# Performance work log

Measured on AMD Instinct MI355X. Metric: run time of the kernel, lower is better.

The kernel has to match this reference:

```python
import jax, jax.numpy as jnp
import numpy as np

B, N, D = 4, 2048, 128
H = 4
HD = D // H          # 32
RL = 4               # rl_dim
BETA = 1.0
TEMPER = 1.0
LN_EPS = 1e-5


def _leaky(x, slope=0.01):
    return jnp.where(x > 0, x, slope * x)


def setup_inputs() -> dict:
    key = jax.random.key(0)
    ks = jax.random.split(key, 12)
    s = 0.05
    return {
        "h":    jax.random.normal(ks[0], (B, N, D), jnp.float32),
        "rh":   jax.random.normal(ks[1], (B, N, RL), jnp.float32),
        "Wl":   jax.random.normal(ks[2], (D, D), jnp.float32) * s,   # linear_l weight [out,in]
        "Wr":   jax.random.normal(ks[3], (D, D), jnp.float32) * s,   # linear_r weight
        "al":   jax.random.normal(ks[4], (HD,), jnp.float32) * s,    # att_l weight (Linear(HD,1))
        "ar":   jax.random.normal(ks[5], (HD,), jnp.float32) * s,    # att_r weight
        "Wrs":  jax.random.normal(ks[6], (RL * H, RL), jnp.float32) * s,  # r_source weight
        "Wrt":  jax.random.normal(ks[7], (RL * H, RL), jnp.float32) * s,  # r_target weight
        "Wf":   jax.random.normal(ks[8], (D, D), jnp.float32) * s,   # linear_final weight
        "ln_g": jnp.ones((D,), jnp.float32),
        "ln_b": jnp.zeros((D,), jnp.float32),
    }


def reference(h, rh, Wl, Wr, al, ar, Wrs, Wrt, Wf, ln_g, ln_b):
    b, n, d = h.shape
    # projections -> [B, H, N, HD]
    fl = (h @ Wl.T).reshape(b, n, H, HD).transpose(0, 2, 1, 3)
    fr = (h @ Wr.T).reshape(b, n, H, HD).transpose(0, 2, 1, 3)
    # rank-1 additive attention scores
    sl = _leaky(fl) @ al                      # [B, H, N]
    sr = _leaky(fr) @ ar                      # [B, H, N]
    score = sl[..., :, None] + sr[..., None, :]  # [B, H, N, N]
    # relational bias: r_k @ r_q
    r_k = (rh @ Wrs.T).reshape(b, n, H, RL).transpose(0, 2, 1, 3)  # [B,H,N,RL]
    r_q = (rh @ Wrt.T).reshape(b, n, H, RL).transpose(0, 2, 3, 1)  # [B,H,RL,N]
    score = score + BETA * jnp.einsum('bhnr,bhrm->bhnm', r_k, r_q)
    attn = jax.nn.softmax(score / TEMPER, axis=-1)
    # context
    ctx = jnp.einsum('bhnm,bhmd->bhnd', attn, fr)  # [B,H,N,HD]
    h_sa = ctx.transpose(0, 2, 1, 3).reshape(b, n, d)
    fh = h_sa @ Wf.T
    # residual + LayerNorm
    x = h + fh
    mu = jnp.mean(x, axis=-1, keepdims=True)
    var = jnp.mean(jnp.square(x - mu), axis=-1, keepdims=True)
    return (x - mu) * jax.lax.rsqrt(var + LN_EPS) * ln_g + ln_b
```

## Files before the change

### kernel.cpp

```cpp
#include <hip/hip_runtime.h>

#define NN 2048
#define DD 128
#define HH 4

typedef __attribute__((ext_vector_type(8))) short short8;
typedef __attribute__((ext_vector_type(16))) float f32x16;
typedef __attribute__((ext_vector_type(4))) unsigned uint4v;

static __device__ __forceinline__ unsigned cvtpk(float lo, float hi) {
  unsigned r;
  asm("v_cvt_pk_bf16_f32 %0, %1, %2" : "=v"(r) : "v"(lo), "v"(hi));
  return r;
}
static __device__ __forceinline__ void plswap(unsigned& a, unsigned& b) {
  asm("v_permlane32_swap_b32 %0, %1" : "+v"(a), "+v"(b));
}
static __device__ __forceinline__ float dot4(float4 a, float4 b) {
  return a.x * b.x + a.y * b.y + a.z * b.z + a.w * b.w;
}

__global__ __launch_bounds__(256) void k1_proj(
    const float* __restrict__ h, const float* __restrict__ Wr,
    const float* __restrict__ ar, short* __restrict__ Vt,
    float* __restrict__ sr) {
  __shared__ short wr_s[DD * DD];
  __shared__ short h_s[32 * DD];
  const int t = threadIdx.x;
  const int lane = t & 63, wv = t >> 6;
  const int b = blockIdx.x >> 6;
  const int j0 = (blockIdx.x & 63) * 32;
  {
    const int d = t >> 1, c0 = (t & 1) * 8;
    const float* src = Wr + d * DD + c0 * 8;
#pragma unroll
    for (int c = 0; c < 8; ++c) {
      const float4 x = *(const float4*)(src + c * 8);
      const float4 y = *(const float4*)(src + c * 8 + 4);
      uint4v v = {cvtpk(x.x, x.y), cvtpk(x.z, x.w), cvtpk(y.x, y.y), cvtpk(y.z, y.w)};
      *(uint4v*)(wr_s + d * DD + (((c0 + c) ^ (d & 7)) << 3)) = v;
    }
  }
  {
    const int j = t >> 3, c0 = (t & 7) * 2;
    const float* src = h + (size_t)(b * NN + j0 + j) * DD + c0 * 8;
#pragma unroll
    for (int c = 0; c < 2; ++c) {
      const float4 x = *(const float4*)(src + c * 8);
      const float4 y = *(const float4*)(src + c * 8 + 4);
      uint4v v = {cvtpk(x.x, x.y), cvtpk(x.z, x.w), cvtpk(y.x, y.y), cvtpk(y.z, y.w)};
      *(uint4v*)(h_s + j * DD + (((c0 + c) ^ (j & 7)) << 3)) = v;
    }
  }
  __syncthreads();
  const int l31 = lane & 31, kg = lane >> 5;
  const int rowA = wv * 32 + l31;
  f32x16 acc = {0, 0, 0, 0, 0, 0, 0, 0, 0, 0, 0, 0, 0, 0, 0, 0};
#pragma unroll
  for (int ks = 0; ks < 8; ++ks) {
    const int ch = ks * 2 + kg;
    const short8 a = *(const short8*)(wr_s + rowA * DD + ((ch ^ (rowA & 7)) << 3));
    const short8 bb = *(const short8*)(h_s + l31 * DD + ((ch ^ (l31 & 7)) << 3));
    acc = __builtin_amdgcn_mfma_f32_32x32x16_bf16(a, bb, acc, 0, 0, 0);
  }
  const int hi4 = kg * 4;
  float4 arv[4];
#pragma unroll
  for (int q = 0; q < 4; ++q) arv[q] = *(const float4*)(ar + q * 8 + hi4);
  float srp = 0.f;
  short* vrow = Vt + (size_t)(b * DD + wv * 32) * NN + j0 + l31;
#pragma unroll
  for (int r = 0; r < 16; ++r) {
    const int dloc = (r & 3) + 8 * (r >> 2) + hi4;
    const float v = acc[r];
    const float lv = v > 0.f ? v : 0.01f * v;
    const float arc =
        (r & 3) == 0 ? arv[r >> 2].x : (r & 3) == 1 ? arv[r >> 2].y : (r & 3) == 2 ? arv[r >> 2].z : arv[r >> 2].w;
    srp += lv * arc;
    vrow[(size_t)dloc * NN] = (short)cvtpk(v, v);
  }
  srp += __shfl_xor(srp, 32);
  if (lane < 32) sr[(b * HH + wv) * NN + j0 + lane] = srp;
}

__global__ __launch_bounds__(256) void k2_attn(
    const float* __restrict__ rh, const float* __restrict__ Wrs,
    const float* __restrict__ Wrt, const float* __restrict__ sr,
    const short* __restrict__ Vt, float* __restrict__ h_sa) {
  __shared__ short rqsr_s[NN * 8];
  __shared__ float4 redA[2][4][64];
  __shared__ float redL[2][64];
  __shared__ float tbuf[2][32 * 36];
  const int t = threadIdx.x;
  const int lane = t & 63, wv = t >> 6;
  const int strip = wv >> 1, jh = wv & 1;
  const int bh = blockIdx.y, b = bh >> 2, head = bh & 3;
  const int i0 = blockIdx.x * 64 + strip * 32;
  const int l31 = lane & 31, kg = lane >> 5;

  const float4 wt0 = *(const float4*)(Wrt + (head * 4 + 0) * 4);
  const float4 wt1 = *(const float4*)(Wrt + (head * 4 + 1) * 4);
  const float4 wt2 = *(const float4*)(Wrt + (head * 4 + 2) * 4);
  const float4 wt3 = *(const float4*)(Wrt + (head * 4 + 3) * 4);
#pragma unroll
  for (int q = 0; q < 8; ++q) {
    const int j = q * 256 + t;
    const float4 r4 = *(const float4*)(rh + (size_t)(b * NN + j) * 4);
    const float srj = sr[bh * NN + j];
    uint4v v = {cvtpk(dot4(r4, wt0), dot4(r4, wt1)), cvtpk(dot4(r4, wt2), dot4(r4, wt3)),
                cvtpk(srj, 0.f), 0u};
    *(uint4v*)(rqsr_s + j * 8) = v;
  }
  uint4v bk = {0u, 0u, 0u, 0u};
  if (lane < 32) {
    const float4 r4 = *(const float4*)(rh + (size_t)(b * NN + i0 + l31) * 4);
    const float4 ws0 = *(const float4*)(Wrs + (head * 4 + 0) * 4);
    const float4 ws1 = *(const float4*)(Wrs + (head * 4 + 1) * 4);
    const float4 ws2 = *(const float4*)(Wrs + (head * 4 + 2) * 4);
    const float4 ws3 = *(const float4*)(Wrs + (head * 4 + 3) * 4);
    bk[0] = cvtpk(dot4(r4, ws0), dot4(r4, ws1));
    bk[1] = cvtpk(dot4(r4, ws2), dot4(r4, ws3));
    bk[2] = cvtpk(1.f, 0.f);
  }
  const short8 bkf = __builtin_bit_cast(short8, bk);
  __syncthreads();

  const short* vtb = Vt + (size_t)bh * 32 * NN + (size_t)l31 * NN;
  const f32x16 zero = {0, 0, 0, 0, 0, 0, 0, 0, 0, 0, 0, 0, 0, 0, 0, 0};
  f32x16 acc = zero;
  float lsum = 0.f;
  const int jbase = jh * 1024;
#pragma unroll 2
  for (int jj = 0; jj < 1024; jj += 32) {
    const int j0w = jbase + jj;
    uint4v aqu = *(const uint4v*)(rqsr_s + (j0w + l31) * 8);
    if (lane >= 32) { aqu[0] = 0u; aqu[1] = 0u; aqu[2] = 0u; aqu[3] = 0u; }
    const short8 aq = __builtin_bit_cast(short8, aqu);
    const f32x16 sc = __builtin_amdgcn_mfma_f32_32x32x16_bf16(aq, bkf, zero, 0, 0, 0);
    float e[16];
#pragma unroll
    for (int r = 0; r < 16; ++r) {
      e[r] = __expf(sc[r]);
      lsum += e[r];
    }
    unsigned d0 = cvtpk(e[0], e[1]), d1 = cvtpk(e[2], e[3]);
    unsigned d2 = cvtpk(e[4], e[5]), d3 = cvtpk(e[6], e[7]);
    unsigned d4 = cvtpk(e[8], e[9]), d5 = cvtpk(e[10], e[11]);
    unsigned d6 = cvtpk(e[12], e[13]), d7 = cvtpk(e[14], e[15]);
    plswap(d0, d2);
    plswap(d1, d3);
    plswap(d4, d6);
    plswap(d5, d7);
    uint4v b0u = {d0, d1, d2, d3};
    uint4v b1u = {d4, d5, d6, d7};
    const short8 p0 = __builtin_bit_cast(short8, b0u);
    const short8 p1 = __builtin_bit_cast(short8, b1u);
    const short8 va0 = *(const short8*)(vtb + j0w + kg * 8);
    const short8 va1 = *(const short8*)(vtb + j0w + 16 + kg * 8);
    acc = __builtin_amdgcn_mfma_f32_32x32x16_bf16(va0, p0, acc, 0, 0, 0);
    acc = __builtin_amdgcn_mfma_f32_32x32x16_bf16(va1, p1, acc, 0, 0, 0);
  }
  lsum += __shfl_xor(lsum, 32);
  if (jh == 1) {
#pragma unroll
    for (int rg = 0; rg < 4; ++rg)
      redA[strip][rg][lane] = make_float4(acc[rg * 4], acc[rg * 4 + 1], acc[rg * 4 + 2], acc[rg * 4 + 3]);
    redL[strip][lane] = lsum;
  }
  __syncthreads();
  if (jh == 0) {
#pragma unroll
    for (int rg = 0; rg < 4; ++rg) {
      const float4 o = redA[strip][rg][lane];
      acc[rg * 4] += o.x;
      acc[rg * 4 + 1] += o.y;
      acc[rg * 4 + 2] += o.z;
      acc[rg * 4 + 3] += o.w;
    }
    lsum += redL[strip][lane];
    const float linv = 1.f / lsum;
    const int hi4 = kg * 4;
#pragma unroll
    for (int r = 0; r < 16; ++r) {
      const int dloc = (r & 3) + 8 * (r >> 2) + hi4;
      tbuf[strip][l31 * 36 + dloc] = acc[r] * linv;
    }
  }
  __syncthreads();
  if (jh == 0) {
    const int il = lane >> 1, hf = lane & 1;
    const float* tp = &tbuf[strip][il * 36 + hf * 16];
    float* op = h_sa + (size_t)(b * NN + i0 + il) * DD + head * 32 + hf * 16;
#pragma unroll
    for (int qq = 0; qq < 4; ++qq) *(float4*)(op + qq * 4) = *(const float4*)(tp + qq * 4);
  }
}

__global__ __launch_bounds__(256) void k3_final(
    const float* __restrict__ h_sa, const float* __restrict__ h,
    const float* __restrict__ Wf, const float* __restrict__ ln_g,
    const float* __restrict__ ln_b, float* __restrict__ out) {
  __shared__ float2 redln[4][32];
  __shared__ float2 fin[32];
  const int t = threadIdx.x, lane = t & 63, wv = t >> 6;
  const int l31 = lane & 31, kg = lane >> 5;
  const int rbase = blockIdx.x * 32, c0 = wv * 32;
  f32x16 acc = {0, 0, 0, 0, 0, 0, 0, 0, 0, 0, 0, 0, 0, 0, 0, 0};
  const float* ap0 = h_sa + (size_t)(rbase + l31) * DD;
  const float* bp0 = Wf + (size_t)(c0 + l31) * DD;
#pragma unroll
  for (int ks = 0; ks < 8; ++ks) {
    const int ko = ks * 16 + kg * 8;
    const float4 a0 = *(const float4*)(ap0 + ko);
    const float4 a1 = *(const float4*)(ap0 + ko + 4);
    const float4 b0 = *(const float4*)(bp0 + ko);
    const float4 b1 = *(const float4*)(bp0 + ko + 4);
    uint4v au = {cvtpk(a0.x, a0.y), cvtpk(a0.z, a0.w), cvtpk(a1.x, a1.y), cvtpk(a1.z, a1.w)};
    uint4v bu = {cvtpk(b0.x, b0.y), cvtpk(b0.z, b0.w), cvtpk(b1.x, b1.y), cvtpk(b1.z, b1.w)};
    acc = __builtin_amdgcn_mfma_f32_32x32x16_bf16(__builtin_bit_cast(short8, au),
                                                  __builtin_bit_cast(short8, bu), acc, 0, 0, 0);
  }
  const int hi4 = kg * 4;
  float x[16];
#pragma unroll
  for (int r = 0; r < 16; ++r) {
    const int row = (r & 3) + 8 * (r >> 2) + hi4;
    x[r] = acc[r] + h[(size_t)(rbase + row) * DD + c0 + l31];
    float a = x[r], bsq = x[r] * x[r];
#pragma unroll
    for (int o = 1; o < 32; o <<= 1) {
      a += __shfl_xor(a, o);
      bsq += __shfl_xor(bsq, o);
    }
    if (l31 == 0) redln[wv][row] = make_float2(a, bsq);
  }
  __syncthreads();
  if (wv == 0 && lane < 32) {
    float ss = 0.f, qq = 0.f;
#pragma unroll
    for (int w = 0; w < 4; ++w) {
      const float2 p = redln[w][lane];
      ss += p.x;
      qq += p.y;
    }
    const float mu = ss * (1.f / 128.f);
    const float var = qq * (1.f / 128.f) - mu * mu;
    fin[lane] = make_float2(mu, rsqrtf(var + 1e-5f));
  }
  __syncthreads();
  const float g = ln_g[c0 + l31], bb = ln_b[c0 + l31];
#pragma unroll
  for (int r = 0; r < 16; ++r) {
    const int row = (r & 3) + 8 * (r >> 2) + hi4;
    const float2 f = fin[row];
    out[(size_t)(rbase + row) * DD + c0 + l31] = (x[r] - f.x) * f.y * g + bb;
  }
}

extern "C" void kernel_launch(void* const* d_in, const int* in_sizes, int n_in,
                              void* d_out, int out_size, void* d_ws, size_t ws_size,
                              hipStream_t stream) {
  (void)in_sizes; (void)n_in; (void)out_size; (void)ws_size;
  const float* h = (const float*)d_in[0];
  const float* rh = (const float*)d_in[1];
  const float* Wr = (const float*)d_in[3];
  const float* ar = (const float*)d_in[5];
  const float* Wrs = (const float*)d_in[6];
  const float* Wrt = (const float*)d_in[7];
  const float* Wf = (const float*)d_in[8];
  const float* ln_g = (const float*)d_in[9];
  const float* ln_b = (const float*)d_in[10];
  float* out = (float*)d_out;

  char* ws = (char*)d_ws;
  short* Vt = (short*)ws;
  float* sr = (float*)(ws + (2u << 20));
  float* h_sa = (float*)(ws + (2u << 20) + (256u << 10));

  hipLaunchKernelGGL(k1_proj, dim3(256), dim3(256), 0, stream, h, Wr, ar, Vt, sr);
  hipLaunchKernelGGL(k2_attn, dim3(32, 16), dim3(256), 0, stream, rh, Wrs, Wrt, sr, Vt, h_sa);
  hipLaunchKernelGGL(k3_final, dim3(256), dim3(256), 0, stream, h_sa, h, Wf, ln_g, ln_b, out);
}
```

Measured before the change: 110.4 us.

## Precompute packed rq/sr in projection kernel and split attention keys across four waves

```diff
diff --git a/kernel.cpp b/kernel.cpp
--- a/kernel.cpp
+++ b/kernel.cpp
@@ -3,6 +3,7 @@
 #define NN 2048
 #define DD 128
 #define HH 4
+#define L2E 1.44269504088896f
 
 typedef __attribute__((ext_vector_type(8))) short short8;
 typedef __attribute__((ext_vector_type(16))) float f32x16;
@@ -22,8 +23,9 @@
 
 __global__ __launch_bounds__(256) void k1_proj(
     const float* __restrict__ h, const float* __restrict__ Wr,
-    const float* __restrict__ ar, short* __restrict__ Vt,
-    float* __restrict__ sr) {
+    const float* __restrict__ ar, const float* __restrict__ rh,
+    const float* __restrict__ Wrt, short* __restrict__ Vt,
+    short* __restrict__ rqsr) {
   __shared__ short wr_s[DD * DD];
   __shared__ short h_s[32 * DD];
   const int t = threadIdx.x;
@@ -80,37 +82,33 @@
     vrow[(size_t)dloc * NN] = (short)cvtpk(v, v);
   }
   srp += __shfl_xor(srp, 32);
-  if (lane < 32) sr[(b * HH + wv) * NN + j0 + lane] = srp;
-}
-
-__global__ __launch_bounds__(256) void k2_attn(
+  if (lane < 32) {
+    const int j = j0 + lane;
+    const float4 r4 = *(const float4*)(rh + (size_t)(b * NN + j) * 4);
+    const float4 wt0 = *(const float4*)(Wrt + (wv * 4 + 0) * 4);
+    const float4 wt1 = *(const float4*)(Wrt + (wv * 4 + 1) * 4);
+    const float4 wt2 = *(const float4*)(Wrt + (wv * 4 + 2) * 4);
+    const float4 wt3 = *(const float4*)(Wrt + (wv * 4 + 3) * 4);
+    uint4v v = {cvtpk(L2E * dot4(r4, wt0), L2E * dot4(r4, wt1)),
+                cvtpk(L2E * dot4(r4, wt2), L2E * dot4(r4, wt3)),
+                cvtpk(L2E * srp, 0.f), 0u};
+    *(uint4v*)(rqsr + ((size_t)(b * HH + wv) * NN + j) * 8) = v;
+  }
+}
+
+__global__ __launch_bounds__(512) void k2_attn(
     const float* __restrict__ rh, const float* __restrict__ Wrs,
-    const float* __restrict__ Wrt, const float* __restrict__ sr,
-    const short* __restrict__ Vt, float* __restrict__ h_sa) {
-  __shared__ short rqsr_s[NN * 8];
-  __shared__ float4 redA[2][4][64];
-  __shared__ float redL[2][64];
+    const short* __restrict__ rqsr, const short* __restrict__ Vt,
+    float* __restrict__ h_sa) {
+  __shared__ float red[2][3][64 * 17];
   __shared__ float tbuf[2][32 * 36];
   const int t = threadIdx.x;
   const int lane = t & 63, wv = t >> 6;
-  const int strip = wv >> 1, jh = wv & 1;
+  const int strip = wv >> 2, jh = wv & 3;
   const int bh = blockIdx.y, b = bh >> 2, head = bh & 3;
   const int i0 = blockIdx.x * 64 + strip * 32;
   const int l31 = lane & 31, kg = lane >> 5;
 
-  const float4 wt0 = *(const float4*)(Wrt + (head * 4 + 0) * 4);
-  const float4 wt1 = *(const float4*)(Wrt + (head * 4 + 1) * 4);
-  const float4 wt2 = *(const float4*)(Wrt + (head * 4 + 2) * 4);
-  const float4 wt3 = *(const float4*)(Wrt + (head * 4 + 3) * 4);
-#pragma unroll
-  for (int q = 0; q < 8; ++q) {
-    const int j = q * 256 + t;
-    const float4 r4 = *(const float4*)(rh + (size_t)(b * NN + j) * 4);
-    const float srj = sr[bh * NN + j];
-    uint4v v = {cvtpk(dot4(r4, wt0), dot4(r4, wt1)), cvtpk(dot4(r4, wt2), dot4(r4, wt3)),
-                cvtpk(srj, 0.f), 0u};
-    *(uint4v*)(rqsr_s + j * 8) = v;
-  }
   uint4v bk = {0u, 0u, 0u, 0u};
   if (lane < 32) {
     const float4 r4 = *(const float4*)(rh + (size_t)(b * NN + i0 + l31) * 4);
@@ -123,26 +121,25 @@
     bk[2] = cvtpk(1.f, 0.f);
   }
   const short8 bkf = __builtin_bit_cast(short8, bk);
-  __syncthreads();
-
-  const short* vtb = Vt + (size_t)bh * 32 * NN + (size_t)l31 * NN;
+
+  const short* vtb = Vt + (size_t)bh * 32 * NN + (size_t)l31 * NN + jh * 512;
+  const short* aqp = rqsr + ((size_t)bh * NN + jh * 512 + l31) * 8;
   const f32x16 zero = {0, 0, 0, 0, 0, 0, 0, 0, 0, 0, 0, 0, 0, 0, 0, 0};
   f32x16 acc = zero;
   float lsum = 0.f;
-  const int jbase = jh * 1024;
-#pragma unroll 2
-  for (int jj = 0; jj < 1024; jj += 32) {
-    const int j0w = jbase + jj;
-    uint4v aqu = *(const uint4v*)(rqsr_s + (j0w + l31) * 8);
-    if (lane >= 32) { aqu[0] = 0u; aqu[1] = 0u; aqu[2] = 0u; aqu[3] = 0u; }
+#pragma unroll 4
+  for (int jj = 0; jj < 512; jj += 32) {
+    const uint4v aqu = *(const uint4v*)(aqp + (size_t)jj * 8);
     const short8 aq = __builtin_bit_cast(short8, aqu);
     const f32x16 sc = __builtin_amdgcn_mfma_f32_32x32x16_bf16(aq, bkf, zero, 0, 0, 0);
     float e[16];
 #pragma unroll
-    for (int r = 0; r < 16; ++r) {
-      e[r] = __expf(sc[r]);
-      lsum += e[r];
-    }
+    for (int r = 0; r < 16; ++r) e[r] = exp2f(sc[r]);
+    const float s0 = (e[0] + e[1]) + (e[2] + e[3]);
+    const float s1 = (e[4] + e[5]) + (e[6] + e[7]);
+    const float s2 = (e[8] + e[9]) + (e[10] + e[11]);
+    const float s3 = (e[12] + e[13]) + (e[14] + e[15]);
+    lsum += (s0 + s1) + (s2 + s3);
     unsigned d0 = cvtpk(e[0], e[1]), d1 = cvtpk(e[2], e[3]);
     unsigned d2 = cvtpk(e[4], e[5]), d3 = cvtpk(e[6], e[7]);
     unsigned d4 = cvtpk(e[8], e[9]), d5 = cvtpk(e[10], e[11]);
@@ -155,29 +152,27 @@
     uint4v b1u = {d4, d5, d6, d7};
     const short8 p0 = __builtin_bit_cast(short8, b0u);
     const short8 p1 = __builtin_bit_cast(short8, b1u);
-    const short8 va0 = *(const short8*)(vtb + j0w + kg * 8);
-    const short8 va1 = *(const short8*)(vtb + j0w + 16 + kg * 8);
+    const short8 va0 = *(const short8*)(vtb + jj + kg * 8);
+    const short8 va1 = *(const short8*)(vtb + jj + 16 + kg * 8);
     acc = __builtin_amdgcn_mfma_f32_32x32x16_bf16(va0, p0, acc, 0, 0, 0);
     acc = __builtin_amdgcn_mfma_f32_32x32x16_bf16(va1, p1, acc, 0, 0, 0);
   }
   lsum += __shfl_xor(lsum, 32);
-  if (jh == 1) {
-#pragma unroll
-    for (int rg = 0; rg < 4; ++rg)
-      redA[strip][rg][lane] = make_float4(acc[rg * 4], acc[rg * 4 + 1], acc[rg * 4 + 2], acc[rg * 4 + 3]);
-    redL[strip][lane] = lsum;
+  if (jh != 0) {
+    float* rp = &red[strip][jh - 1][lane * 17];
+#pragma unroll
+    for (int r = 0; r < 16; ++r) rp[r] = acc[r];
+    rp[16] = lsum;
   }
   __syncthreads();
   if (jh == 0) {
 #pragma unroll
-    for (int rg = 0; rg < 4; ++rg) {
-      const float4 o = redA[strip][rg][lane];
-      acc[rg * 4] += o.x;
-      acc[rg * 4 + 1] += o.y;
-      acc[rg * 4 + 2] += o.z;
-      acc[rg * 4 + 3] += o.w;
-    }
-    lsum += redL[strip][lane];
+    for (int s = 0; s < 3; ++s) {
+      const float* rp = &red[strip][s][lane * 17];
+#pragma unroll
+      for (int r = 0; r < 16; ++r) acc[r] += rp[r];
+      lsum += rp[16];
+    }
     const float linv = 1.f / lsum;
     const int hi4 = kg * 4;
 #pragma unroll
@@ -185,9 +180,6 @@
       const int dloc = (r & 3) + 8 * (r >> 2) + hi4;
       tbuf[strip][l31 * 36 + dloc] = acc[r] * linv;
     }
-  }
-  __syncthreads();
-  if (jh == 0) {
     const int il = lane >> 1, hf = lane & 1;
     const float* tp = &tbuf[strip][il * 36 + hf * 16];
     float* op = h_sa + (size_t)(b * NN + i0 + il) * DD + head * 32 + hf * 16;
@@ -274,10 +266,10 @@
 
   char* ws = (char*)d_ws;
   short* Vt = (short*)ws;
-  float* sr = (float*)(ws + (2u << 20));
-  float* h_sa = (float*)(ws + (2u << 20) + (256u << 10));
-
-  hipLaunchKernelGGL(k1_proj, dim3(256), dim3(256), 0, stream, h, Wr, ar, Vt, sr);
-  hipLaunchKernelGGL(k2_attn, dim3(32, 16), dim3(256), 0, stream, rh, Wrs, Wrt, sr, Vt, h_sa);
+  short* rqsr = (short*)(ws + (2u << 20));
+  float* h_sa = (float*)(ws + (3u << 20));
+
+  hipLaunchKernelGGL(k1_proj, dim3(256), dim3(256), 0, stream, h, Wr, ar, rh, Wrt, Vt, rqsr);
+  hipLaunchKernelGGL(k2_attn, dim3(32, 16), dim3(512), 0, stream, rh, Wrs, rqsr, Vt, h_sa);
   hipLaunchKernelGGL(k3_final, dim3(256), dim3(256), 0, stream, h_sa, h, Wf, ln_g, ln_b, out);
 }
```

Result: slower. 115.6 us (+4.7%).
